# Kernel tuning notes

Hardware: AMD Instinct MI355X
Metric: run time of the kernel (lower is better)

Reference implementation:

```python
import jax, jax.numpy as jnp
import numpy as np

N_SAMPLES = 128
AGENTS = 64
D = 128          # latent_size
EDIM = 2         # edge attr dim
N = N_SAMPLES * AGENTS
EPS = 1e-5


def _build_edges():
    a = np.arange(AGENTS)
    rows = np.repeat(a, AGENTS)
    cols = np.tile(a, AGENTS)
    mask = rows != cols  # fully connected, no self loops
    rows, cols = rows[mask], cols[mask]
    offsets = (np.arange(N_SAMPLES) * AGENTS)[:, None]
    src = (rows[None, :] + offsets).ravel().astype(np.int32)  # edge_index[0]
    dst = (cols[None, :] + offsets).ravel().astype(np.int32)  # edge_index[1]
    return src, dst


def setup_inputs() -> dict:
    key = jax.random.key(0)
    ks = jax.random.split(key, 16)
    src, dst = _build_edges()
    zin = 2 * D + EDIM  # CGConv concat [x_i, x_j, e]
    inp = {
        "gnn_in": jax.random.normal(ks[0], (N, D), jnp.float32),
        "centers": jax.random.normal(ks[1], (N, EDIM), jnp.float32),
        "edge_src": jnp.asarray(src),
        "edge_dst": jnp.asarray(dst),
    }
    for li, base in ((1, 2), (2, 8)):
        inp[f"Wf{li}"] = jax.random.normal(ks[base + 0], (zin, D), jnp.float32) / np.sqrt(zin)
        inp[f"bf{li}"] = jnp.zeros((D,), jnp.float32)
        inp[f"Ws{li}"] = jax.random.normal(ks[base + 1], (zin, D), jnp.float32) / np.sqrt(zin)
        inp[f"bs{li}"] = jnp.zeros((D,), jnp.float32)
        inp[f"gamma{li}"] = jnp.ones((D,), jnp.float32)
        inp[f"beta{li}"] = jnp.zeros((D,), jnp.float32)
    return inp


def _cgconv(x, e, src, dst, Wf, bf, Ws, bs, gamma, beta):
    # message: z = [x_i(target), x_j(source), e]; sigmoid(Wf z) * softplus(Ws z)
    z = jnp.concatenate([x[dst], x[src], e], axis=-1)  # [E, 2D+2]
    m = jax.nn.sigmoid(z @ Wf + bf) * jax.nn.softplus(z @ Ws + bs)
    agg = jax.ops.segment_sum(m, dst, num_segments=N)  # scatter-add at targets
    # batch norm (training-mode batch stats) then residual, as in PyG CGConv
    mu = agg.mean(axis=0)
    var = agg.var(axis=0)
    agg = (agg - mu) * jax.lax.rsqrt(var + EPS) * gamma + beta
    return agg + x


def reference(gnn_in, centers, edge_src, edge_dst,
              Wf1, bf1, Ws1, bs1, gamma1, beta1,
              Wf2, bf2, Ws2, bs2, gamma2, beta2):
    # edge_attr = centers[col] - centers[row]
    e = centers[edge_dst] - centers[edge_src]  # [E, 2]
    x = jax.nn.relu(_cgconv(gnn_in, e, edge_src, edge_dst, Wf1, bf1, Ws1, bs1, gamma1, beta1))
    x = jax.nn.relu(_cgconv(x, e, edge_src, edge_dst, Wf2, bf2, Ws2, bs2, gamma2, beta2))
    return x
```

## Files before the change

kernel.cpp:

```cpp
#include <hip/hip_runtime.h>
#include <hip/hip_bf16.h>

#define NSAMP 128
#define AGENTS 64
#define D 128
#define NN (NSAMP * AGENTS)
#define LOG2E 1.44269504088896340736f
#define LN2   0.69314718055994530942f
#define EPSF  1e-5f

__global__ __launch_bounds__(256) void prep_kernel(
    const float* __restrict__ x,
    const float* __restrict__ centers,
    const float* __restrict__ Wf,
    const float* __restrict__ bf,
    const float* __restrict__ Ws,
    const float* __restrict__ bs,
    float* __restrict__ out)
{
    const int mt  = blockIdx.x >> 3;
    const int nt  = blockIdx.x & 7;
    const int arr = nt >> 1;
    const int c0  = (nt & 1) * 64;
    const float* Wsrc = (arr < 2) ? Wf : Ws;
    const int rowoff = (arr & 1) ? D : 0;
    const int m0 = mt * 64;
    const int tid = threadIdx.x;

    __shared__ float Xs[64][132];
    __shared__ float Wt[128][64];

    #pragma unroll
    for (int i = 0; i < 8; ++i) {
        int f4 = i * 256 + tid;
        int idx = f4 * 4;
        int m = idx >> 7, k = idx & 127;
        float4 v = *(const float4*)&x[(size_t)(m0 + m) * D + k];
        *(float4*)&Xs[m][k] = v;
    }
    #pragma unroll
    for (int i = 0; i < 8; ++i) {
        int f4 = i * 256 + tid;
        int idx = f4 * 4;
        int k = idx >> 6, lc = idx & 63;
        float4 v = *(const float4*)&Wsrc[(size_t)(rowoff + k) * D + c0 + lc];
        *(float4*)&Wt[k][lc] = v;
    }
    __syncthreads();

    const int tr = tid >> 4;
    const int tc = tid & 15;

    float acc[4][4] = {};
    for (int k = 0; k < D; k += 4) {
        float4 a[4], w[4];
        #pragma unroll
        for (int im = 0; im < 4; ++im) a[im] = *(const float4*)&Xs[tr * 4 + im][k];
        #pragma unroll
        for (int kk = 0; kk < 4; ++kk) w[kk] = *(const float4*)&Wt[k + kk][tc * 4];
        #pragma unroll
        for (int im = 0; im < 4; ++im) {
            const float* ap = (const float*)&a[im];
            #pragma unroll
            for (int kk = 0; kk < 4; ++kk) {
                const float* wp = (const float*)&w[kk];
                float av = ap[kk];
                acc[im][0] = fmaf(av, wp[0], acc[im][0]);
                acc[im][1] = fmaf(av, wp[1], acc[im][1]);
                acc[im][2] = fmaf(av, wp[2], acc[im][2]);
                acc[im][3] = fmaf(av, wp[3], acc[im][3]);
            }
        }
    }

    const float sgn   = (arr & 1) ? -1.f : 1.f;
    const float scale = (arr < 2) ? -LOG2E : LOG2E;
    float cw0[4], cw1[4], bias[4];
    #pragma unroll
    for (int jn = 0; jn < 4; ++jn) {
        int c = c0 + tc * 4 + jn;
        cw0[jn] = Wsrc[256 * D + c];
        cw1[jn] = Wsrc[257 * D + c];
        bias[jn] = (arr == 0) ? bf[c] : ((arr == 2) ? bs[c] : 0.f);
    }
    float* obase = out + (size_t)arr * NN * D;
    #pragma unroll
    for (int im = 0; im < 4; ++im) {
        int n = m0 + tr * 4 + im;
        float ce0 = centers[2 * n], ce1 = centers[2 * n + 1];
        float4 v;
        float* vp = (float*)&v;
        #pragma unroll
        for (int jn = 0; jn < 4; ++jn) {
            float t = acc[im][jn] + bias[jn] + sgn * fmaf(ce0, cw0[jn], ce1 * cw1[jn]);
            vp[jn] = __builtin_amdgcn_exp2f(scale * t);
        }
        *(float4*)&obase[(size_t)n * D + c0 + tc * 4] = v;
    }
}

__global__ __launch_bounds__(256) void edge_kernel(
    const float* __restrict__ EAf, const float* __restrict__ EBf,
    const float* __restrict__ EAs, const float* __restrict__ EBs,
    float* __restrict__ agg,
    float* __restrict__ partials)
{
    const int s = blockIdx.x >> 2;
    const int g = blockIdx.x & 3;
    const int tid = threadIdx.x;
    const int c  = tid & 127;
    const int dh = tid >> 7;
    const int nbase = s * AGENTS;

    __shared__ float Bfs[AGENTS][D];
    __shared__ float Bss[AGENTS][D];

    #pragma unroll
    for (int i = 0; i < 8; ++i) {
        int f4 = i * 256 + tid;
        int idx = f4 * 4;
        int j = idx >> 7, cc = idx & 127;
        *(float4*)&Bfs[j][cc] = *(const float4*)&EBf[(size_t)(nbase + j) * D + cc];
        *(float4*)&Bss[j][cc] = *(const float4*)&EBs[(size_t)(nbase + j) * D + cc];
    }
    __syncthreads();

    const int d0 = g * 16 + dh * 8;
    float eaf[8], eas[8], acc[8];
    #pragma unroll
    for (int i = 0; i < 8; ++i) {
        int n = nbase + d0 + i;
        eaf[i] = EAf[(size_t)n * D + c];
        eas[i] = EAs[(size_t)n * D + c];
        acc[i] = 0.f;
    }

    for (int j = 0; j < AGENTS; ++j) {
        float ebf = Bfs[j][c];
        float ebs = Bss[j][c];
        #pragma unroll
        for (int i = 0; i < 8; ++i) {
            float sg = __builtin_amdgcn_rcpf(1.f + eaf[i] * ebf);
            float lg = __builtin_amdgcn_logf(1.f + eas[i] * ebs);
            acc[i] += sg * lg;
        }
    }

    float s1 = 0.f, s2 = 0.f;
    #pragma unroll
    for (int i = 0; i < 8; ++i) {
        int j = d0 + i;
        float sg = __builtin_amdgcn_rcpf(1.f + eaf[i] * Bfs[j][c]);
        float lg = __builtin_amdgcn_logf(1.f + eas[i] * Bss[j][c]);
        float a = (acc[i] - sg * lg) * LN2;
        agg[(size_t)(nbase + d0 + i) * D + c] = a;
        s1 += a;
        s2 += a * a;
    }

    __syncthreads();
    if (dh == 1) { Bfs[0][c] = s1; Bss[0][c] = s2; }
    __syncthreads();
    if (dh == 0) {
        s1 += Bfs[0][c];
        s2 += Bss[0][c];
        partials[(size_t)blockIdx.x * 256 + c]       = s1;
        partials[(size_t)blockIdx.x * 256 + 128 + c] = s2;
    }
}

__global__ __launch_bounds__(256) void stats_kernel(
    const float* __restrict__ partials, float* __restrict__ stats)
{
    const int c = blockIdx.x;
    const int t = threadIdx.x;
    float s1 = partials[(size_t)t * 256 + c] + partials[(size_t)(t + 256) * 256 + c];
    float s2 = partials[(size_t)t * 256 + 128 + c] + partials[(size_t)(t + 256) * 256 + 128 + c];
    __shared__ float r1[256], r2[256];
    r1[t] = s1; r2[t] = s2;
    __syncthreads();
    for (int off = 128; off > 0; off >>= 1) {
        if (t < off) { r1[t] += r1[t + off]; r2[t] += r2[t + off]; }
        __syncthreads();
    }
    if (t == 0) {
        float mu = r1[0] * (1.f / NN);
        float var = r2[0] * (1.f / NN) - mu * mu;
        stats[c]     = mu;
        stats[D + c] = rsqrtf(var + EPSF);
    }
}

__global__ __launch_bounds__(256) void bn_kernel(
    const float* __restrict__ agg, const float* __restrict__ xin,
    const float* __restrict__ stats,
    const float* __restrict__ gamma, const float* __restrict__ beta,
    float* __restrict__ outp)
{
    const int t = blockIdx.x * 256 + threadIdx.x;
    const int n = t >> 5;
    const int c = (t & 31) * 4;
    float4 a  = *(const float4*)&agg[(size_t)n * D + c];
    float4 xv = *(const float4*)&xin[(size_t)n * D + c];
    float4 mu = *(const float4*)&stats[c];
    float4 rs = *(const float4*)&stats[D + c];
    float4 gm = *(const float4*)&gamma[c];
    float4 bt = *(const float4*)&beta[c];
    float4 o;
    o.x = fmaxf(0.f, fmaf((a.x - mu.x) * rs.x, gm.x, bt.x) + xv.x);
    o.y = fmaxf(0.f, fmaf((a.y - mu.y) * rs.y, gm.y, bt.y) + xv.y);
    o.z = fmaxf(0.f, fmaf((a.z - mu.z) * rs.z, gm.z, bt.z) + xv.z);
    o.w = fmaxf(0.f, fmaf((a.w - mu.w) * rs.w, gm.w, bt.w) + xv.w);
    *(float4*)&outp[(size_t)n * D + c] = o;
}

extern "C" void kernel_launch(void* const* d_in, const int* in_sizes, int n_in,
                              void* d_out, int out_size, void* d_ws, size_t ws_size,
                              hipStream_t stream) {
    const float* x0      = (const float*)d_in[0];
    const float* centers = (const float*)d_in[1];
    const float* Wf[2] = { (const float*)d_in[4],  (const float*)d_in[10] };
    const float* bf[2] = { (const float*)d_in[5],  (const float*)d_in[11] };
    const float* Ws[2] = { (const float*)d_in[6],  (const float*)d_in[12] };
    const float* bs[2] = { (const float*)d_in[7],  (const float*)d_in[13] };
    const float* gm[2] = { (const float*)d_in[8],  (const float*)d_in[14] };
    const float* bt[2] = { (const float*)d_in[9],  (const float*)d_in[15] };

    float* ws       = (float*)d_ws;
    const size_t ND = (size_t)NN * D;
    float* AB       = ws;
    float* agg      = ws + 4 * ND;
    float* x1       = ws + 5 * ND;
    float* partials = ws + 6 * ND;
    float* stats    = partials + 512 * 256;

    float* outp = (float*)d_out;

    const float* xin = x0;
    for (int l = 0; l < 2; ++l) {
        float* xout = (l == 0) ? x1 : outp;
        prep_kernel<<<dim3(1024), dim3(256), 0, stream>>>(
            xin, centers, Wf[l], bf[l], Ws[l], bs[l], AB);
        edge_kernel<<<dim3(512), dim3(256), 0, stream>>>(
            AB, AB + ND, AB + 2 * ND, AB + 3 * ND, agg, partials);
        stats_kernel<<<dim3(128), dim3(256), 0, stream>>>(partials, stats);
        bn_kernel<<<dim3(1024), dim3(256), 0, stream>>>(
            agg, xin, stats, gm[l], bt[l], xout);
        xin = x1;
    }
}
```

Before: 180.0 us.

## Fuse layer-1 batchnorm+ReLU into layer-2 prep and enlarge prep GEMM tiles

The first layer's batchnorm, residual and ReLU are now applied while layer 2's prep kernel loads its input tile, and x1 is written out only by the arr==0 blocks. This removes one bn_kernel launch and a full read/write pass over the activations. Separately, the prep kernel now computes a 128x128 output tile per block with 8x8 accumulators per thread. That cuts the grid from 1024 to 256 blocks and reduces redundant loads of X and W. In exchange, each block uses about 130KB of LDS and more registers, which limits occupancy to roughly one block per CU.

```diff
diff --git a/kernel.cpp b/kernel.cpp
--- a/kernel.cpp
+++ b/kernel.cpp
@@ -16,87 +16,120 @@
     const float* __restrict__ bf,
     const float* __restrict__ Ws,
     const float* __restrict__ bs,
+    const float* __restrict__ agg,
+    const float* __restrict__ stats,
+    const float* __restrict__ gamma, const float* __restrict__ beta,
+    float* __restrict__ x1out,
     float* __restrict__ out)
 {
-    const int mt  = blockIdx.x >> 3;
-    const int nt  = blockIdx.x & 7;
-    const int arr = nt >> 1;
-    const int c0  = (nt & 1) * 64;
-    const float* Wsrc = (arr < 2) ? Wf : Ws;
-    const int rowoff = (arr & 1) ? D : 0;
-    const int m0 = mt * 64;
+    const int mt  = blockIdx.x >> 2;
+    const int arr = blockIdx.x & 3;
+    const int m0  = mt * 128;
     const int tid = threadIdx.x;
-
-    __shared__ float Xs[64][132];
-    __shared__ float Wt[128][64];
-
-    #pragma unroll
-    for (int i = 0; i < 8; ++i) {
+    const float* Wsrc  = (arr < 2) ? Wf : Ws;
+    const int    rowoff = (arr & 1) ? D : 0;
+    const bool   fuse  = (agg != nullptr);
+
+    __shared__ float Xs[128][132];
+    __shared__ float Wt[128][128];
+
+    #pragma unroll
+    for (int i = 0; i < 16; ++i) {
         int f4 = i * 256 + tid;
         int idx = f4 * 4;
         int m = idx >> 7, k = idx & 127;
-        float4 v = *(const float4*)&x[(size_t)(m0 + m) * D + k];
+        size_t goff = (size_t)(m0 + m) * D + k;
+        float4 v = *(const float4*)&x[goff];
+        if (fuse) {
+            float4 a  = *(const float4*)&agg[goff];
+            float4 mu = *(const float4*)&stats[k];
+            float4 rs = *(const float4*)&stats[D + k];
+            float4 gm = *(const float4*)&gamma[k];
+            float4 bt = *(const float4*)&beta[k];
+            v.x = fmaxf(0.f, fmaf((a.x - mu.x) * rs.x, gm.x, bt.x) + v.x);
+            v.y = fmaxf(0.f, fmaf((a.y - mu.y) * rs.y, gm.y, bt.y) + v.y);
+            v.z = fmaxf(0.f, fmaf((a.z - mu.z) * rs.z, gm.z, bt.z) + v.z);
+            v.w = fmaxf(0.f, fmaf((a.w - mu.w) * rs.w, gm.w, bt.w) + v.w);
+            if (arr == 0) *(float4*)&x1out[goff] = v;
+        }
         *(float4*)&Xs[m][k] = v;
     }
     #pragma unroll
-    for (int i = 0; i < 8; ++i) {
+    for (int i = 0; i < 16; ++i) {
         int f4 = i * 256 + tid;
         int idx = f4 * 4;
-        int k = idx >> 6, lc = idx & 63;
-        float4 v = *(const float4*)&Wsrc[(size_t)(rowoff + k) * D + c0 + lc];
-        *(float4*)&Wt[k][lc] = v;
+        int k = idx >> 7, c = idx & 127;
+        *(float4*)&Wt[k][c] = *(const float4*)&Wsrc[(size_t)(rowoff + k) * D + c];
     }
     __syncthreads();
 
     const int tr = tid >> 4;
     const int tc = tid & 15;
 
-    float acc[4][4] = {};
+    float acc[8][8] = {};
     for (int k = 0; k < D; k += 4) {
-        float4 a[4], w[4];
-        #pragma unroll
-        for (int im = 0; im < 4; ++im) a[im] = *(const float4*)&Xs[tr * 4 + im][k];
-        #pragma unroll
-        for (int kk = 0; kk < 4; ++kk) w[kk] = *(const float4*)&Wt[k + kk][tc * 4];
+        float4 a0[4], a1[4], w0[4], w1[4];
         #pragma unroll
         for (int im = 0; im < 4; ++im) {
-            const float* ap = (const float*)&a[im];
+            a0[im] = *(const float4*)&Xs[tr * 4 + im][k];
+            a1[im] = *(const float4*)&Xs[64 + tr * 4 + im][k];
+        }
+        #pragma unroll
+        for (int kk = 0; kk < 4; ++kk) {
+            w0[kk] = *(const float4*)&Wt[k + kk][tc * 4];
+            w1[kk] = *(const float4*)&Wt[k + kk][64 + tc * 4];
+        }
+        #pragma unroll
+        for (int im = 0; im < 4; ++im) {
+            const float* ap0 = (const float*)&a0[im];
+            const float* ap1 = (const float*)&a1[im];
             #pragma unroll
             for (int kk = 0; kk < 4; ++kk) {
-                const float* wp = (const float*)&w[kk];
-                float av = ap[kk];
-                acc[im][0] = fmaf(av, wp[0], acc[im][0]);
-                acc[im][1] = fmaf(av, wp[1], acc[im][1]);
-                acc[im][2] = fmaf(av, wp[2], acc[im][2]);
-                acc[im][3] = fmaf(av, wp[3], acc[im][3]);
+                const float* wp0 = (const float*)&w0[kk];
+                const float* wp1 = (const float*)&w1[kk];
+                float av0 = ap0[kk], av1 = ap1[kk];
+                #pragma unroll
+                for (int jn = 0; jn < 4; ++jn) {
+                    acc[im][jn]         = fmaf(av0, wp0[jn], acc[im][jn]);
+                    acc[im][jn + 4]     = fmaf(av0, wp1[jn], acc[im][jn + 4]);
+                    acc[im + 4][jn]     = fmaf(av1, wp0[jn], acc[im + 4][jn]);
+                    acc[im + 4][jn + 4] = fmaf(av1, wp1[jn], acc[im + 4][jn + 4]);
+                }
             }
         }
     }
 
     const float sgn   = (arr & 1) ? -1.f : 1.f;
     const float scale = (arr < 2) ? -LOG2E : LOG2E;
-    float cw0[4], cw1[4], bias[4];
-    #pragma unroll
-    for (int jn = 0; jn < 4; ++jn) {
-        int c = c0 + tc * 4 + jn;
-        cw0[jn] = Wsrc[256 * D + c];
-        cw1[jn] = Wsrc[257 * D + c];
-        bias[jn] = (arr == 0) ? bf[c] : ((arr == 2) ? bs[c] : 0.f);
-    }
+    float cw0[2][4], cw1[2][4], bias[2][4];
+    #pragma unroll
+    for (int cg = 0; cg < 2; ++cg)
+        #pragma unroll
+        for (int jn = 0; jn < 4; ++jn) {
+            int c = cg * 64 + tc * 4 + jn;
+            cw0[cg][jn] = Wsrc[256 * D + c];
+            cw1[cg][jn] = Wsrc[257 * D + c];
+            bias[cg][jn] = (arr == 0) ? bf[c] : ((arr == 2) ? bs[c] : 0.f);
+        }
     float* obase = out + (size_t)arr * NN * D;
     #pragma unroll
-    for (int im = 0; im < 4; ++im) {
-        int n = m0 + tr * 4 + im;
-        float ce0 = centers[2 * n], ce1 = centers[2 * n + 1];
-        float4 v;
-        float* vp = (float*)&v;
-        #pragma unroll
-        for (int jn = 0; jn < 4; ++jn) {
-            float t = acc[im][jn] + bias[jn] + sgn * fmaf(ce0, cw0[jn], ce1 * cw1[jn]);
-            vp[jn] = __builtin_amdgcn_exp2f(scale * t);
-        }
-        *(float4*)&obase[(size_t)n * D + c0 + tc * 4] = v;
-    }
+    for (int rg = 0; rg < 2; ++rg)
+        #pragma unroll
+        for (int im = 0; im < 4; ++im) {
+            int n = m0 + rg * 64 + tr * 4 + im;
+            float ce0 = centers[2 * n], ce1 = centers[2 * n + 1];
+            #pragma unroll
+            for (int cg = 0; cg < 2; ++cg) {
+                float4 v; float* vp = (float*)&v;
+                #pragma unroll
+                for (int jn = 0; jn < 4; ++jn) {
+                    float t = acc[rg * 4 + im][cg * 4 + jn] + bias[cg][jn]
+                            + sgn * fmaf(ce0, cw0[cg][jn], ce1 * cw1[cg][jn]);
+                    vp[jn] = __builtin_amdgcn_exp2f(scale * t);
+                }
+                *(float4*)&obase[(size_t)n * D + cg * 64 + tc * 4] = v;
+            }
+        }
 }
 
 __global__ __launch_bounds__(256) void edge_kernel(
@@ -236,16 +269,18 @@
 
     float* outp = (float*)d_out;
 
-    const float* xin = x0;
-    for (int l = 0; l < 2; ++l) {
-        float* xout = (l == 0) ? x1 : outp;
-        prep_kernel<<<dim3(1024), dim3(256), 0, stream>>>(
-            xin, centers, Wf[l], bf[l], Ws[l], bs[l], AB);
-        edge_kernel<<<dim3(512), dim3(256), 0, stream>>>(
-            AB, AB + ND, AB + 2 * ND, AB + 3 * ND, agg, partials);
-        stats_kernel<<<dim3(128), dim3(256), 0, stream>>>(partials, stats);
-        bn_kernel<<<dim3(1024), dim3(256), 0, stream>>>(
-            agg, xin, stats, gm[l], bt[l], xout);
-        xin = x1;
-    }
-}
+    prep_kernel<<<dim3(256), dim3(256), 0, stream>>>(
+        x0, centers, Wf[0], bf[0], Ws[0], bs[0],
+        nullptr, nullptr, nullptr, nullptr, nullptr, AB);
+    edge_kernel<<<dim3(512), dim3(256), 0, stream>>>(
+        AB, AB + ND, AB + 2 * ND, AB + 3 * ND, agg, partials);
+    stats_kernel<<<dim3(128), dim3(256), 0, stream>>>(partials, stats);
+    prep_kernel<<<dim3(256), dim3(256), 0, stream>>>(
+        x0, centers, Wf[1], bf[1], Ws[1], bs[1],
+        agg, stats, gm[0], bt[0], x1, AB);
+    edge_kernel<<<dim3(512), dim3(256), 0, stream>>>(
+        AB, AB + ND, AB + 2 * ND, AB + 3 * ND, agg, partials);
+    stats_kernel<<<dim3(128), dim3(256), 0, stream>>>(partials, stats);
+    bn_kernel<<<dim3(1024), dim3(256), 0, stream>>>(
+        agg, x1, stats, gm[1], bt[1], outp);
+}
```

After: 186.1 us. 1.03x slower.

## Use bf16 MFMA for node projections and store exp tables in bf16

Applied to the files above, without the earlier changes.

Replaces the fp32 FMA tiled GEMM in the per-node projection with bf16 MFMA 16x16x32 instructions. Inputs and transposed weights are converted to bf16 in a new conversion kernel, and the first-layer batch-norm kernel now also writes a bf16 copy of the activations. The four exponentiated projection tables are stored as bf16, halving the traffic the edge kernel reads. The cost is bf16 rounding in the matmul and in the exp tables, plus an extra conversion launch.

```diff
diff --git a/kernel.cpp b/kernel.cpp
--- a/kernel.cpp
+++ b/kernel.cpp
@@ -9,99 +9,110 @@
 #define LN2   0.69314718055994530942f
 #define EPSF  1e-5f
 
-__global__ __launch_bounds__(256) void prep_kernel(
-    const float* __restrict__ x,
+typedef __attribute__((ext_vector_type(8))) short short8;
+typedef __attribute__((ext_vector_type(4))) float floatx4;
+
+__device__ __forceinline__ float bf2f(unsigned short u) {
+    unsigned v = ((unsigned)u) << 16;
+    float f; __builtin_memcpy(&f, &v, 4); return f;
+}
+__device__ __forceinline__ unsigned short f2bf(float f) {
+    unsigned x; __builtin_memcpy(&x, &f, 4);
+    return (unsigned short)((x + 0x7FFFu + ((x >> 16) & 1u)) >> 16);
+}
+
+__global__ __launch_bounds__(256) void cvt_kernel(
+    const float* __restrict__ x0,
+    const float* __restrict__ Wf1, const float* __restrict__ Ws1,
+    const float* __restrict__ Wf2, const float* __restrict__ Ws2,
+    unsigned short* __restrict__ Xb, unsigned short* __restrict__ WT)
+{
+    int b = blockIdx.x;
+    if (b < 512) {
+        int off = (b * 256 + threadIdx.x) * 8;
+        float4 v0 = *(const float4*)&x0[off];
+        float4 v1 = *(const float4*)&x0[off + 4];
+        short8 s;
+        s[0] = (short)f2bf(v0.x); s[1] = (short)f2bf(v0.y);
+        s[2] = (short)f2bf(v0.z); s[3] = (short)f2bf(v0.w);
+        s[4] = (short)f2bf(v1.x); s[5] = (short)f2bf(v1.y);
+        s[6] = (short)f2bf(v1.z); s[7] = (short)f2bf(v1.w);
+        *(short8*)&Xb[off] = s;
+    } else {
+        int wb = b - 512;
+        int rr = wb * 16 + (threadIdx.x >> 4);
+        int kk = (threadIdx.x & 15) * 8;
+        int layer = rr >> 9, rem = rr & 511, arr = rem >> 7, c = rem & 127;
+        const float* M = (arr < 2) ? (layer ? Wf2 : Wf1) : (layer ? Ws2 : Ws1);
+        int side = arr & 1;
+        short8 s;
+        #pragma unroll
+        for (int j = 0; j < 8; ++j)
+            s[j] = (short)f2bf(M[(size_t)(side * 128 + kk + j) * D + c]);
+        *(short8*)&WT[(size_t)(layer * 4 + arr) * 16384 + c * 128 + kk] = s;
+    }
+}
+
+__global__ __launch_bounds__(256) void prep_mfma(
+    const unsigned short* __restrict__ Xb,
+    const unsigned short* __restrict__ WT,
     const float* __restrict__ centers,
-    const float* __restrict__ Wf,
-    const float* __restrict__ bf,
-    const float* __restrict__ Ws,
-    const float* __restrict__ bs,
-    float* __restrict__ out)
-{
-    const int mt  = blockIdx.x >> 3;
-    const int nt  = blockIdx.x & 7;
-    const int arr = nt >> 1;
-    const int c0  = (nt & 1) * 64;
-    const float* Wsrc = (arr < 2) ? Wf : Ws;
-    const int rowoff = (arr & 1) ? D : 0;
-    const int m0 = mt * 64;
-    const int tid = threadIdx.x;
-
-    __shared__ float Xs[64][132];
-    __shared__ float Wt[128][64];
-
-    #pragma unroll
-    for (int i = 0; i < 8; ++i) {
-        int f4 = i * 256 + tid;
-        int idx = f4 * 4;
-        int m = idx >> 7, k = idx & 127;
-        float4 v = *(const float4*)&x[(size_t)(m0 + m) * D + k];
-        *(float4*)&Xs[m][k] = v;
-    }
-    #pragma unroll
-    for (int i = 0; i < 8; ++i) {
-        int f4 = i * 256 + tid;
-        int idx = f4 * 4;
-        int k = idx >> 6, lc = idx & 63;
-        float4 v = *(const float4*)&Wsrc[(size_t)(rowoff + k) * D + c0 + lc];
-        *(float4*)&Wt[k][lc] = v;
-    }
-    __syncthreads();
-
-    const int tr = tid >> 4;
-    const int tc = tid & 15;
-
-    float acc[4][4] = {};
-    for (int k = 0; k < D; k += 4) {
-        float4 a[4], w[4];
-        #pragma unroll
-        for (int im = 0; im < 4; ++im) a[im] = *(const float4*)&Xs[tr * 4 + im][k];
-        #pragma unroll
-        for (int kk = 0; kk < 4; ++kk) w[kk] = *(const float4*)&Wt[k + kk][tc * 4];
-        #pragma unroll
-        for (int im = 0; im < 4; ++im) {
-            const float* ap = (const float*)&a[im];
-            #pragma unroll
-            for (int kk = 0; kk < 4; ++kk) {
-                const float* wp = (const float*)&w[kk];
-                float av = ap[kk];
-                acc[im][0] = fmaf(av, wp[0], acc[im][0]);
-                acc[im][1] = fmaf(av, wp[1], acc[im][1]);
-                acc[im][2] = fmaf(av, wp[2], acc[im][2]);
-                acc[im][3] = fmaf(av, wp[3], acc[im][3]);
-            }
+    const float* __restrict__ Wf, const float* __restrict__ bf_,
+    const float* __restrict__ Ws, const float* __restrict__ bs_,
+    unsigned short* __restrict__ out)
+{
+    const int m0   = blockIdx.x * 16;
+    const int wv   = threadIdx.x >> 6;
+    const int lane = threadIdx.x & 63;
+    const int quad = lane >> 4, l16 = lane & 15;
+
+    short8 a[4];
+    const unsigned short* xrow = Xb + (size_t)(m0 + l16) * 128 + quad * 8;
+    #pragma unroll
+    for (int kc = 0; kc < 4; ++kc) a[kc] = *(const short8*)(xrow + kc * 32);
+
+    float ce0[4], ce1[4];
+    #pragma unroll
+    for (int r = 0; r < 4; ++r) {
+        int n = m0 + quad * 4 + r;
+        ce0[r] = centers[2 * n]; ce1[r] = centers[2 * n + 1];
+    }
+
+    const float sgn   = (wv & 1) ? -1.f : 1.f;
+    const float scale = (wv < 2) ? -LOG2E : LOG2E;
+    const float* Wsrc = (wv < 2) ? Wf : Ws;
+    const float* bias = (wv == 0) ? bf_ : ((wv == 2) ? bs_ : nullptr);
+    const unsigned short* Wa = WT + (size_t)wv * 16384;
+    unsigned short* ob = out + (size_t)wv * NN * 128;
+
+    for (int nt = 0; nt < 8; ++nt) {
+        const int n0 = nt * 16;
+        short8 bfr[4];
+        const unsigned short* wrow = Wa + (size_t)(n0 + l16) * 128 + quad * 8;
+        #pragma unroll
+        for (int kc = 0; kc < 4; ++kc) bfr[kc] = *(const short8*)(wrow + kc * 32);
+
+        floatx4 acc = {0.f, 0.f, 0.f, 0.f};
+        #pragma unroll
+        for (int kc = 0; kc < 4; ++kc)
+            acc = __builtin_amdgcn_mfma_f32_16x16x32_bf16(a[kc], bfr[kc], acc, 0, 0, 0);
+
+        const int col = n0 + l16;
+        const float cw0 = Wsrc[256 * D + col];
+        const float cw1 = Wsrc[257 * D + col];
+        const float bv  = bias ? bias[col] : 0.f;
+        #pragma unroll
+        for (int r = 0; r < 4; ++r) {
+            float t = acc[r] + bv + sgn * fmaf(ce0[r], cw0, ce1[r] * cw1);
+            ob[(size_t)(m0 + quad * 4 + r) * 128 + col] =
+                f2bf(__builtin_amdgcn_exp2f(scale * t));
         }
     }
-
-    const float sgn   = (arr & 1) ? -1.f : 1.f;
-    const float scale = (arr < 2) ? -LOG2E : LOG2E;
-    float cw0[4], cw1[4], bias[4];
-    #pragma unroll
-    for (int jn = 0; jn < 4; ++jn) {
-        int c = c0 + tc * 4 + jn;
-        cw0[jn] = Wsrc[256 * D + c];
-        cw1[jn] = Wsrc[257 * D + c];
-        bias[jn] = (arr == 0) ? bf[c] : ((arr == 2) ? bs[c] : 0.f);
-    }
-    float* obase = out + (size_t)arr * NN * D;
-    #pragma unroll
-    for (int im = 0; im < 4; ++im) {
-        int n = m0 + tr * 4 + im;
-        float ce0 = centers[2 * n], ce1 = centers[2 * n + 1];
-        float4 v;
-        float* vp = (float*)&v;
-        #pragma unroll
-        for (int jn = 0; jn < 4; ++jn) {
-            float t = acc[im][jn] + bias[jn] + sgn * fmaf(ce0, cw0[jn], ce1 * cw1[jn]);
-            vp[jn] = __builtin_amdgcn_exp2f(scale * t);
-        }
-        *(float4*)&obase[(size_t)n * D + c0 + tc * 4] = v;
-    }
 }
 
 __global__ __launch_bounds__(256) void edge_kernel(
-    const float* __restrict__ EAf, const float* __restrict__ EBf,
-    const float* __restrict__ EAs, const float* __restrict__ EBs,
+    const unsigned short* __restrict__ EAf, const unsigned short* __restrict__ EBf,
+    const unsigned short* __restrict__ EAs, const unsigned short* __restrict__ EBs,
     float* __restrict__ agg,
     float* __restrict__ partials)
 {
@@ -116,12 +127,25 @@
     __shared__ float Bss[AGENTS][D];
 
     #pragma unroll
-    for (int i = 0; i < 8; ++i) {
-        int f4 = i * 256 + tid;
-        int idx = f4 * 4;
+    for (int i = 0; i < 4; ++i) {
+        int f8 = i * 256 + tid;
+        int idx = f8 * 8;
         int j = idx >> 7, cc = idx & 127;
-        *(float4*)&Bfs[j][cc] = *(const float4*)&EBf[(size_t)(nbase + j) * D + cc];
-        *(float4*)&Bss[j][cc] = *(const float4*)&EBs[(size_t)(nbase + j) * D + cc];
+        short8 vf = *(const short8*)&EBf[(size_t)(nbase + j) * D + cc];
+        short8 vs = *(const short8*)&EBs[(size_t)(nbase + j) * D + cc];
+        float4 f0, f1, s0, s1v;
+        f0.x = bf2f((unsigned short)vf[0]); f0.y = bf2f((unsigned short)vf[1]);
+        f0.z = bf2f((unsigned short)vf[2]); f0.w = bf2f((unsigned short)vf[3]);
+        f1.x = bf2f((unsigned short)vf[4]); f1.y = bf2f((unsigned short)vf[5]);
+        f1.z = bf2f((unsigned short)vf[6]); f1.w = bf2f((unsigned short)vf[7]);
+        s0.x = bf2f((unsigned short)vs[0]); s0.y = bf2f((unsigned short)vs[1]);
+        s0.z = bf2f((unsigned short)vs[2]); s0.w = bf2f((unsigned short)vs[3]);
+        s1v.x = bf2f((unsigned short)vs[4]); s1v.y = bf2f((unsigned short)vs[5]);
+        s1v.z = bf2f((unsigned short)vs[6]); s1v.w = bf2f((unsigned short)vs[7]);
+        *(float4*)&Bfs[j][cc]     = f0;
+        *(float4*)&Bfs[j][cc + 4] = f1;
+        *(float4*)&Bss[j][cc]     = s0;
+        *(float4*)&Bss[j][cc + 4] = s1v;
     }
     __syncthreads();
 
@@ -130,8 +154,8 @@
     #pragma unroll
     for (int i = 0; i < 8; ++i) {
         int n = nbase + d0 + i;
-        eaf[i] = EAf[(size_t)n * D + c];
-        eas[i] = EAs[(size_t)n * D + c];
+        eaf[i] = bf2f(EAf[(size_t)n * D + c]);
+        eas[i] = bf2f(EAs[(size_t)n * D + c]);
         acc[i] = 0.f;
     }
 
@@ -189,6 +213,37 @@
         stats[c]     = mu;
         stats[D + c] = rsqrtf(var + EPSF);
     }
+}
+
+__global__ __launch_bounds__(256) void bncvt_kernel(
+    const float* __restrict__ agg, const float* __restrict__ xin,
+    const float* __restrict__ stats,
+    const float* __restrict__ gamma, const float* __restrict__ beta,
+    float* __restrict__ x1, unsigned short* __restrict__ Xb)
+{
+    const int t = blockIdx.x * 256 + threadIdx.x;
+    const int n = t >> 4;
+    const int c = (t & 15) * 8;
+    size_t off = (size_t)n * D + c;
+    float v[8]; short8 s;
+    #pragma unroll
+    for (int h = 0; h < 2; ++h) {
+        float4 a  = *(const float4*)&agg[off + h * 4];
+        float4 xv = *(const float4*)&xin[off + h * 4];
+        float4 mu = *(const float4*)&stats[c + h * 4];
+        float4 rs = *(const float4*)&stats[D + c + h * 4];
+        float4 gm = *(const float4*)&gamma[c + h * 4];
+        float4 bt = *(const float4*)&beta[c + h * 4];
+        v[h*4+0] = fmaxf(0.f, fmaf((a.x - mu.x) * rs.x, gm.x, bt.x) + xv.x);
+        v[h*4+1] = fmaxf(0.f, fmaf((a.y - mu.y) * rs.y, gm.y, bt.y) + xv.y);
+        v[h*4+2] = fmaxf(0.f, fmaf((a.z - mu.z) * rs.z, gm.z, bt.z) + xv.z);
+        v[h*4+3] = fmaxf(0.f, fmaf((a.w - mu.w) * rs.w, gm.w, bt.w) + xv.w);
+    }
+    *(float4*)&x1[off]     = *(float4*)&v[0];
+    *(float4*)&x1[off + 4] = *(float4*)&v[4];
+    #pragma unroll
+    for (int e = 0; e < 8; ++e) s[e] = (short)f2bf(v[e]);
+    *(short8*)&Xb[off] = s;
 }
 
 __global__ __launch_bounds__(256) void bn_kernel(
@@ -226,26 +281,35 @@
     const float* gm[2] = { (const float*)d_in[8],  (const float*)d_in[14] };
     const float* bt[2] = { (const float*)d_in[9],  (const float*)d_in[15] };
 
-    float* ws       = (float*)d_ws;
     const size_t ND = (size_t)NN * D;
-    float* AB       = ws;
-    float* agg      = ws + 4 * ND;
-    float* x1       = ws + 5 * ND;
-    float* partials = ws + 6 * ND;
+    unsigned short* ws_u = (unsigned short*)d_ws;
+    unsigned short* Xb = ws_u;
+    unsigned short* WT = ws_u + ND;
+    unsigned short* AB = WT + 2 * 65536;
+    float* fbase    = (float*)(AB + 4 * ND);
+    float* agg      = fbase;
+    float* x1       = fbase + ND;
+    float* partials = fbase + 2 * ND;
     float* stats    = partials + 512 * 256;
 
     float* outp = (float*)d_out;
 
-    const float* xin = x0;
-    for (int l = 0; l < 2; ++l) {
-        float* xout = (l == 0) ? x1 : outp;
-        prep_kernel<<<dim3(1024), dim3(256), 0, stream>>>(
-            xin, centers, Wf[l], bf[l], Ws[l], bs[l], AB);
-        edge_kernel<<<dim3(512), dim3(256), 0, stream>>>(
-            AB, AB + ND, AB + 2 * ND, AB + 3 * ND, agg, partials);
-        stats_kernel<<<dim3(128), dim3(256), 0, stream>>>(partials, stats);
-        bn_kernel<<<dim3(1024), dim3(256), 0, stream>>>(
-            agg, xin, stats, gm[l], bt[l], xout);
-        xin = x1;
-    }
-}
+    cvt_kernel<<<dim3(576), dim3(256), 0, stream>>>(
+        x0, Wf[0], Ws[0], Wf[1], Ws[1], Xb, WT);
+
+    prep_mfma<<<dim3(512), dim3(256), 0, stream>>>(
+        Xb, WT, centers, Wf[0], bf[0], Ws[0], bs[0], AB);
+    edge_kernel<<<dim3(512), dim3(256), 0, stream>>>(
+        AB, AB + ND, AB + 2 * ND, AB + 3 * ND, agg, partials);
+    stats_kernel<<<dim3(128), dim3(256), 0, stream>>>(partials, stats);
+    bncvt_kernel<<<dim3(512), dim3(256), 0, stream>>>(
+        agg, x0, stats, gm[0], bt[0], x1, Xb);
+
+    prep_mfma<<<dim3(512), dim3(256), 0, stream>>>(
+        Xb, WT + 65536, centers, Wf[1], bf[1], Ws[1], bs[1], AB);
+    edge_kernel<<<dim3(512), dim3(256), 0, stream>>>(
+        AB, AB + ND, AB + 2 * ND, AB + 3 * ND, agg, partials);
+    stats_kernel<<<dim3(128), dim3(256), 0, stream>>>(partials, stats);
+    bn_kernel<<<dim3(1024), dim3(256), 0, stream>>>(
+        agg, x1, stats, gm[1], bt[1], outp);
+}
```

After: 165.2 us. 8.2% less time.
